# Performance work log

Hardware: AMD Instinct MI355X
Metric: run time of the kernel (lower is better)

Reference implementation:

```python
import jax, jax.numpy as jnp
import numpy as np

B, H, W = 64, 512, 512
HS = (3, 3)  # h_shape


def setup_inputs() -> dict:
    key = jax.random.key(0)
    k1, k2 = jax.random.split(key)
    x = jax.random.normal(k1, (B, H, W), dtype=jnp.float32)
    # filter param: fixed 1.0 at [0,0], small trainable values elsewhere
    w = 0.01 * jax.random.normal(k2, HS, dtype=jnp.float32)
    w = w.at[0, 0].set(1.0)
    return {"x": x, "w": w}


def reference(x, w):
    # pad input by H/4, W/4 on each side of the last two dims
    ph, pw = x.shape[-2] // 4, x.shape[-1] // 4
    xm = jnp.pad(x, ((0, 0), (ph, ph), (pw, pw)))
    Hp, Wp = xm.shape[-2], xm.shape[-1]
    # zero-pad small filter to the padded grid (top-left corner)
    hm1 = jnp.pad(w, ((0, Hp - w.shape[-2]), (0, Wp - w.shape[-1])))
    # frequency-domain reciprocal filter, shape [Hp, Wp//2+1]
    gm1f = 1.0 / jnp.fft.rfft2(hm1)
    gm2f = jnp.roll(gm1f[::-1, :], shift=1, axis=0)
    gm3f = jnp.roll(gm1f[:, ::-1], shift=1, axis=1)
    gm4f = jnp.roll(gm3f[::-1, :], shift=1, axis=0)
    gmf = (gm1f * gm2f) * (gm3f * gm4f)
    # apply in frequency domain and invert
    ymf = gmf[None, :, :] * jnp.fft.rfft2(xm)
    ym = jnp.fft.irfft2(ymf, s=(Hp, Wp))
    return ym
```

## Files before the change

kernel.cpp:

```cpp
#include <hip/hip_runtime.h>

#define HP   768
#define NV   385
#define HIN  512
#define WIN  512
#define K    8
#define A    17
#define PADO 136
#define TW   64
#define TH   64
#define LH   80
#define LWL  80
#define LWS  84
#define HROWS 40
#define HSIZE (HROWS * LWS)

#define OB   120
#define OE   648
#define NT9  9
#define ACT0_Q 30
#define ACT1_Q 174

#define TWO_PI_OVER_HP 0.008181230868723419f

typedef float f4v __attribute__((ext_vector_type(4)));

__device__ inline float2 cmul(float2 a, float2 b) {
    return make_float2(a.x*b.x - a.y*b.y, a.x*b.y + a.y*b.x);
}

__device__ inline float2 evalF_t(int u, int v, const float* w9,
                                 const float2* __restrict__ tbl) {
    float fr = 0.f, fi = 0.f;
#pragma unroll
    for (int i = 0; i < 3; ++i) {
#pragma unroll
        for (int j = 0; j < 3; ++j) {
            int idx = u * i + v * j;
            if (idx >= 2 * HP) idx -= 2 * HP;
            if (idx >= HP)     idx -= HP;
            float2 e = tbl[idx];
            float wv = w9[i * 3 + j];
            fr += wv * e.x;
            fi -= wv * e.y;
        }
    }
    return make_float2(fr, fi);
}

__global__ __launch_bounds__(320) void filt_P_kernel(
        const float* __restrict__ w, float2* __restrict__ P) {
    __shared__ float2 tbl[HP];
    __shared__ float2 lg[HP];
    __shared__ float2 red[20][16];
    int v = blockIdx.x;
    int tid = threadIdx.x;

    float w9[9];
#pragma unroll
    for (int i = 0; i < 9; ++i) w9[i] = w[i];

    for (int m = tid; m < HP; m += 320) {
        float s, c;
        sincosf((float)m * TWO_PI_OVER_HP, &s, &c);
        tbl[m] = make_float2(c, s);
    }
    __syncthreads();

    int sv = (v == 0) ? 0 : (NV - v);
    for (int u = tid; u < HP; u += 320) {
        int su = (HP - u) % HP;
        float2 F1 = evalF_t(u,  v,  w9, tbl);
        float2 F2 = evalF_t(su, v,  w9, tbl);
        float2 F3 = evalF_t(u,  sv, w9, tbl);
        float2 F4 = evalF_t(su, sv, w9, tbl);
        float2 pr = cmul(cmul(F1, F2), cmul(F3, F4));
        float d = pr.x * pr.x + pr.y * pr.y;
        lg[u] = make_float2(pr.x / d, -pr.y / d);
    }
    __syncthreads();

    int a   = tid >> 4;
    int sub = tid & 15;
    if (a < A) {
        int ap  = a - K;
        int apu = (ap < 0) ? ap + HP : ap;
        float Pr = 0.f, Pi = 0.f;
        for (int u = sub; u < HP; u += 16) {
            int idx = (u * apu) % HP;
            float2 e = tbl[idx];
            float2 g = lg[u];
            Pr += g.x * e.x - g.y * e.y;
            Pi += g.x * e.y + g.y * e.x;
        }
        red[a][sub] = make_float2(Pr, Pi);
    }
    __syncthreads();
    if (tid < A) {
        float Pr = 0.f, Pi = 0.f;
#pragma unroll
        for (int s2 = 0; s2 < 16; ++s2) { Pr += red[tid][s2].x; Pi += red[tid][s2].y; }
        P[tid * NV + v] = make_float2(Pr, Pi);
    }
}

__global__ __launch_bounds__(320) void filt_gk_kernel(
        const float2* __restrict__ P, float* __restrict__ gkf) {
    __shared__ float2 tbl[HP];
    __shared__ float2 Prow[NV];
    __shared__ float  red[20][16];
    int ai  = blockIdx.x;
    int tid = threadIdx.x;

    for (int m = tid; m < HP; m += 320) {
        float s, c;
        sincosf((float)m * TWO_PI_OVER_HP, &s, &c);
        tbl[m] = make_float2(c, s);
    }
    for (int m = tid; m < NV; m += 320)
        Prow[m] = P[ai * NV + m];
    __syncthreads();

    int bi  = tid >> 4;
    int sub = tid & 15;
    if (bi < A) {
        int bp  = bi - K;
        int bpu = (bp < 0) ? bp + HP : bp;
        float sum = 0.f;
        for (int vv = sub; vv < NV; vv += 16) {
            float wv = (vv == 0 || vv == NV - 1) ? 1.f : 2.f;
            int idx = (vv * bpu) % HP;
            float2 e = tbl[idx];
            float2 p = Prow[vv];
            sum += wv * (p.x * e.x - p.y * e.y);
        }
        red[bi][sub] = sum;
    }
    __syncthreads();
    if (tid < A) {
        float s = 0.f;
#pragma unroll
        for (int s2 = 0; s2 < 16; ++s2) s += red[tid][s2];
        gkf[(2 * K - ai) * A + (2 * K - tid)] = s * (1.f / ((float)HP * (float)HP));
    }
}

__global__ __launch_bounds__(256) void zero_border_kernel(float* __restrict__ out) {
    int gid  = blockIdx.x;
    int img  = gid / 192;
    int rg   = gid - img * 192;
    int lane = threadIdx.x & 63;
    int w    = threadIdx.x >> 6;
    int row  = rg * 4 + w;
    f4v* base = (f4v*)(out + ((size_t)img * HP + row) * HP);
    f4v z = {0.f, 0.f, 0.f, 0.f};
    if (row >= OB && row < OB + NT9 * TH) {
        if (lane < ACT0_Q)
            __builtin_nontemporal_store(z, base + lane);
        else if (lane < ACT0_Q + (192 - ACT1_Q))
            __builtin_nontemporal_store(z, base + ACT1_Q + (lane - ACT0_Q));
    } else {
        __builtin_nontemporal_store(z, base + lane);
        __builtin_nontemporal_store(z, base + lane + 64);
        __builtin_nontemporal_store(z, base + lane + 128);
    }
}

__global__ __launch_bounds__(256, 4) void deconv_kernel(
        const float* __restrict__ x, const float* __restrict__ gkf,
        float* __restrict__ out) {
    __shared__ __align__(16) float tile[2 * HSIZE];

    const int tx = threadIdx.x;
    const int ty = threadIdx.y;
    const int tid = ty * 8 + tx;
    const int bx = blockIdx.x, by = blockIdx.y, bz = blockIdx.z;

    const int ix0 = bx * TW + (OB - PADO);
    const int iy0 = by * TH + (OB - PADO);
    const int oy0 = OB + by * TH + ty * 2;
    const int ox0 = OB + bx * TW + tx * 8;
    float* orow0 = out + ((size_t)bz * HP + oy0) * HP + ox0;
    float* orow1 = orow0 + HP;

    const float* xb = x + (size_t)bz * (HIN * WIN);
    for (int l = tid; l < LH * (LWL / 4); l += 256) {
        int r = l / 20, c4 = l - r * 20;
        int gy = iy0 + r;
        int gx = ix0 + c4 * 4;
        f4v val = {0.f, 0.f, 0.f, 0.f};
        if ((unsigned)gy < (unsigned)HIN && (unsigned)gx < (unsigned)WIN)
            val = *(const f4v*)&xb[gy * WIN + gx];
        *(f4v*)&tile[(r & 1) * HSIZE + (r >> 1) * LWS + c4 * 4] = val;
    }
    __syncthreads();

    if (oy0 >= OE) {
        f4v z = {0.f, 0.f, 0.f, 0.f};
        __builtin_nontemporal_store(z, (f4v*)orow0);
        __builtin_nontemporal_store(z, (f4v*)orow0 + 1);
        __builtin_nontemporal_store(z, (f4v*)orow1);
        __builtin_nontemporal_store(z, (f4v*)orow1 + 1);
        return;
    }

    const float* tE = tile;
    const float* tO = tile + HSIZE;

    float accA[8], accB[8];
#pragma unroll
    for (int c = 0; c < 8; ++c) { accA[c] = 0.f; accB[c] = 0.f; }

    f4v rbA[6], rbB[6];

    auto loadRow = [&](f4v* rb, const float* tb, int rowp) {
        const float* p = tb + rowp * LWS + tx * 8;
#pragma unroll
        for (int q = 0; q < 6; ++q)
            rb[q] = *(const f4v*)&p[q * 4];
    };
    auto fmaRow = [&](const float* gp, const f4v* r, float* acc) {
#pragma unroll
        for (int bb = 0; bb < A; ++bb) {
            float g = gp[bb];
#pragma unroll
            for (int c = 0; c < 8; ++c) {
                int i = bb + c;
                acc[c] += g * r[i >> 2][i & 3];
            }
        }
    };

    loadRow(rbA, tE, ty);
#pragma unroll 1
    for (int aa = 0; aa < 16; aa += 2) {
        int h = aa >> 1;
        loadRow(rbB, tO, ty + h);
        fmaRow(gkf + aa * A, rbA, accA);
        fmaRow(gkf + aa * A, rbB, accB);
        loadRow(rbA, tE, ty + h + 1);
        fmaRow(gkf + (aa + 1) * A, rbB, accA);
        fmaRow(gkf + (aa + 1) * A, rbA, accB);
    }
    loadRow(rbB, tO, ty + 8);
    fmaRow(gkf + 16 * A, rbA, accA);
    fmaRow(gkf + 16 * A, rbB, accB);

    f4v vA0 = {accA[0], accA[1], accA[2], accA[3]};
    f4v vA1 = {accA[4], accA[5], accA[6], accA[7]};
    f4v vB0 = {accB[0], accB[1], accB[2], accB[3]};
    f4v vB1 = {accB[4], accB[5], accB[6], accB[7]};
    __builtin_nontemporal_store(vA0, (f4v*)orow0);
    __builtin_nontemporal_store(vA1, (f4v*)orow0 + 1);
    __builtin_nontemporal_store(vB0, (f4v*)orow1);
    __builtin_nontemporal_store(vB1, (f4v*)orow1 + 1);
}

extern "C" void kernel_launch(void* const* d_in, const int* in_sizes, int n_in,
                              void* d_out, int out_size, void* d_ws, size_t ws_size,
                              hipStream_t stream) {
    const float* x = (const float*)d_in[0];
    const float* w = (const float*)d_in[1];
    float* out = (float*)d_out;

    float2* P   = (float2*)d_ws;
    float*  gkf = (float*)d_ws + (size_t)A * NV * 2;

    filt_P_kernel<<<dim3(NV), dim3(320), 0, stream>>>(w, P);
    filt_gk_kernel<<<dim3(A), dim3(320), 0, stream>>>(P, gkf);
    zero_border_kernel<<<dim3(64 * 192), dim3(256), 0, stream>>>(out);
    deconv_kernel<<<dim3(NT9, NT9, 64), dim3(8, 32), 0, stream>>>(x, gkf, out);
}
```

Baseline: 307.2 us.

## Compute four output rows per thread to raise smem row reuse in deconv

Each thread now produces four consecutive output rows instead of two. The block shrinks to 128 threads and the shared tile is split into four interleaved row phases. Each shared-memory row load is reused across up to four accumulator sets, which cuts LDS traffic per FMA. In exchange it needs more registers (32 accumulators) and occupancy drops, with launch bounds going from 4 to 3 per CU. Each block also keeps the same shared tile while running half as many threads.

```diff
diff --git a/kernel.cpp b/kernel.cpp
--- a/kernel.cpp
+++ b/kernel.cpp
@@ -12,8 +12,8 @@
 #define LH   80
 #define LWL  80
 #define LWS  84
-#define HROWS 40
-#define HSIZE (HROWS * LWS)
+#define SUBROWS 20
+#define SUBSIZE (SUBROWS * LWS)
 
 #define OB   120
 #define OE   648
@@ -166,10 +166,10 @@
     }
 }
 
-__global__ __launch_bounds__(256, 4) void deconv_kernel(
+__global__ __launch_bounds__(128, 3) void deconv_kernel(
         const float* __restrict__ x, const float* __restrict__ gkf,
         float* __restrict__ out) {
-    __shared__ __align__(16) float tile[2 * HSIZE];
+    __shared__ __align__(16) float tile[4 * SUBSIZE];
 
     const int tx = threadIdx.x;
     const int ty = threadIdx.y;
@@ -178,48 +178,47 @@
 
     const int ix0 = bx * TW + (OB - PADO);
     const int iy0 = by * TH + (OB - PADO);
-    const int oy0 = OB + by * TH + ty * 2;
+    const int oy0 = OB + by * TH + ty * 4;
     const int ox0 = OB + bx * TW + tx * 8;
-    float* orow0 = out + ((size_t)bz * HP + oy0) * HP + ox0;
-    float* orow1 = orow0 + HP;
+    float* orow = out + ((size_t)bz * HP + oy0) * HP + ox0;
 
     const float* xb = x + (size_t)bz * (HIN * WIN);
-    for (int l = tid; l < LH * (LWL / 4); l += 256) {
+    for (int l = tid; l < LH * (LWL / 4); l += 128) {
         int r = l / 20, c4 = l - r * 20;
         int gy = iy0 + r;
         int gx = ix0 + c4 * 4;
         f4v val = {0.f, 0.f, 0.f, 0.f};
         if ((unsigned)gy < (unsigned)HIN && (unsigned)gx < (unsigned)WIN)
             val = *(const f4v*)&xb[gy * WIN + gx];
-        *(f4v*)&tile[(r & 1) * HSIZE + (r >> 1) * LWS + c4 * 4] = val;
+        *(f4v*)&tile[(r & 3) * SUBSIZE + (r >> 2) * LWS + c4 * 4] = val;
     }
     __syncthreads();
 
     if (oy0 >= OE) {
         f4v z = {0.f, 0.f, 0.f, 0.f};
-        __builtin_nontemporal_store(z, (f4v*)orow0);
-        __builtin_nontemporal_store(z, (f4v*)orow0 + 1);
-        __builtin_nontemporal_store(z, (f4v*)orow1);
-        __builtin_nontemporal_store(z, (f4v*)orow1 + 1);
+#pragma unroll
+        for (int j = 0; j < 4; ++j) {
+            __builtin_nontemporal_store(z, (f4v*)(orow + j * HP));
+            __builtin_nontemporal_store(z, (f4v*)(orow + j * HP) + 1);
+        }
         return;
     }
 
-    const float* tE = tile;
-    const float* tO = tile + HSIZE;
-
-    float accA[8], accB[8];
-#pragma unroll
-    for (int c = 0; c < 8; ++c) { accA[c] = 0.f; accB[c] = 0.f; }
-
-    f4v rbA[6], rbB[6];
-
-    auto loadRow = [&](f4v* rb, const float* tb, int rowp) {
-        const float* p = tb + rowp * LWS + tx * 8;
+    float acc0[8], acc1[8], acc2[8], acc3[8];
+#pragma unroll
+    for (int c = 0; c < 8; ++c) { acc0[c] = 0.f; acc1[c] = 0.f; acc2[c] = 0.f; acc3[c] = 0.f; }
+
+    f4v rbX[6], rbY[6];
+    const float* tlane = tile + ty * LWS + tx * 8;
+
+    auto loadRow = [&](f4v* rb, int p) {
+        const float* ptr = tlane + (p & 3) * SUBSIZE + (p >> 2) * LWS;
 #pragma unroll
         for (int q = 0; q < 6; ++q)
-            rb[q] = *(const f4v*)&p[q * 4];
+            rb[q] = *(const f4v*)&ptr[q * 4];
     };
-    auto fmaRow = [&](const float* gp, const f4v* r, float* acc) {
+    auto fmaRow = [&](int a, const f4v* r, float* acc) {
+        const float* gp = gkf + a * A;
 #pragma unroll
         for (int bb = 0; bb < A; ++bb) {
             float g = gp[bb];
@@ -231,29 +230,50 @@
         }
     };
 
-    loadRow(rbA, tE, ty);
+    loadRow(rbX, 0);
+    loadRow(rbY, 1);
+    fmaRow(0, rbX, acc0);
+    loadRow(rbX, 2);
+    fmaRow(1, rbY, acc0);
+    fmaRow(0, rbY, acc1);
+    loadRow(rbY, 3);
+    fmaRow(2, rbX, acc0);
+    fmaRow(1, rbX, acc1);
+    fmaRow(0, rbX, acc2);
+
 #pragma unroll 1
-    for (int aa = 0; aa < 16; aa += 2) {
-        int h = aa >> 1;
-        loadRow(rbB, tO, ty + h);
-        fmaRow(gkf + aa * A, rbA, accA);
-        fmaRow(gkf + aa * A, rbB, accB);
-        loadRow(rbA, tE, ty + h + 1);
-        fmaRow(gkf + (aa + 1) * A, rbB, accA);
-        fmaRow(gkf + (aa + 1) * A, rbA, accB);
-    }
-    loadRow(rbB, tO, ty + 8);
-    fmaRow(gkf + 16 * A, rbA, accA);
-    fmaRow(gkf + 16 * A, rbB, accB);
-
-    f4v vA0 = {accA[0], accA[1], accA[2], accA[3]};
-    f4v vA1 = {accA[4], accA[5], accA[6], accA[7]};
-    f4v vB0 = {accB[0], accB[1], accB[2], accB[3]};
-    f4v vB1 = {accB[4], accB[5], accB[6], accB[7]};
-    __builtin_nontemporal_store(vA0, (f4v*)orow0);
-    __builtin_nontemporal_store(vA1, (f4v*)orow0 + 1);
-    __builtin_nontemporal_store(vB0, (f4v*)orow1);
-    __builtin_nontemporal_store(vB1, (f4v*)orow1 + 1);
+    for (int pp = 3; pp <= 15; pp += 2) {
+        loadRow(rbX, pp + 1);
+        fmaRow(pp,     rbY, acc0);
+        fmaRow(pp - 1, rbY, acc1);
+        fmaRow(pp - 2, rbY, acc2);
+        fmaRow(pp - 3, rbY, acc3);
+        loadRow(rbY, pp + 2);
+        fmaRow(pp + 1, rbX, acc0);
+        fmaRow(pp,     rbX, acc1);
+        fmaRow(pp - 1, rbX, acc2);
+        fmaRow(pp - 2, rbX, acc3);
+    }
+
+    fmaRow(16, rbY, acc1);
+    fmaRow(15, rbY, acc2);
+    fmaRow(14, rbY, acc3);
+    loadRow(rbX, 18);
+    fmaRow(16, rbX, acc2);
+    fmaRow(15, rbX, acc3);
+    loadRow(rbY, 19);
+    fmaRow(16, rbY, acc3);
+
+    auto st = [&](const float* acc, float* row) {
+        f4v v0 = {acc[0], acc[1], acc[2], acc[3]};
+        f4v v1 = {acc[4], acc[5], acc[6], acc[7]};
+        __builtin_nontemporal_store(v0, (f4v*)row);
+        __builtin_nontemporal_store(v1, (f4v*)row + 1);
+    };
+    st(acc0, orow);
+    st(acc1, orow + HP);
+    st(acc2, orow + 2 * HP);
+    st(acc3, orow + 3 * HP);
 }
 
 extern "C" void kernel_launch(void* const* d_in, const int* in_sizes, int n_in,
@@ -269,5 +289,5 @@
     filt_P_kernel<<<dim3(NV), dim3(320), 0, stream>>>(w, P);
     filt_gk_kernel<<<dim3(A), dim3(320), 0, stream>>>(P, gkf);
     zero_border_kernel<<<dim3(64 * 192), dim3(256), 0, stream>>>(out);
-    deconv_kernel<<<dim3(NT9, NT9, 64), dim3(8, 32), 0, stream>>>(x, gkf, out);
-}
+    deconv_kernel<<<dim3(NT9, NT9, 64), dim3(8, 16), 0, stream>>>(x, gkf, out);
+}
```

Measured after the change: 309.1 us. About the same (+0.6%).
